# Optimization experiments

Measured on AMD Instinct MI355X. Metric: run time of the kernel, lower is better.

## Reference

```python
import jax, jax.numpy as jnp
import numpy as np

D_MODEL = 1024
NUM_HEADS = 16


def setup_inputs() -> dict:
    key = jax.random.key(0)
    ks = jax.random.split(key, 11)
    B, L, D = 1, 4096, D_MODEL
    s = 1.0 / np.sqrt(D)
    inp = {
        "Q": jax.random.normal(ks[0], (B, L, D), jnp.float32),
        "K": jax.random.normal(ks[1], (B, L, D), jnp.float32),
        "V": jax.random.normal(ks[2], (B, L, D), jnp.float32),
        "w_q": jax.random.normal(ks[3], (D, D), jnp.float32) * s,
        "b_q": jax.random.normal(ks[4], (D,), jnp.float32) * s,
        "w_k": jax.random.normal(ks[5], (D, D), jnp.float32) * s,
        "b_k": jax.random.normal(ks[6], (D,), jnp.float32) * s,
        "w_v": jax.random.normal(ks[7], (D, D), jnp.float32) * s,
        "b_v": jax.random.normal(ks[8], (D,), jnp.float32) * s,
        "w_o": jax.random.normal(ks[9], (D, D), jnp.float32) * s,
        "b_o": jax.random.normal(ks[10], (D,), jnp.float32) * s,
    }
    return inp


def _split_heads(x, n_heads):
    B, L, D = x.shape
    return x.reshape(B, L, n_heads, D // n_heads).transpose(0, 2, 1, 3)  # (B,H,L,Dh)


def reference(Q, K, V, w_q, b_q, w_k, b_k, w_v, b_v, w_o, b_o):
    H = NUM_HEADS
    # QKV projections (torch Linear: x @ W.T + b)
    q = _split_heads(Q @ w_q.T + b_q, H)
    k = _split_heads(K @ w_k.T + b_k, H)
    v = _split_heads(V @ w_v.T + b_v, H)
    d_h = q.shape[-1]
    scores = jnp.einsum("bhqd,bhkd->bhqk", q, k) / jnp.sqrt(jnp.float32(d_h))
    attn = jax.nn.softmax(scores, axis=-1)
    out = jnp.einsum("bhqk,bhkd->bhqd", attn, v)  # (B,H,L,Dh)
    B, _, L, _ = out.shape
    out = out.transpose(0, 2, 1, 3).reshape(B, L, H * d_h)
    return out @ w_o.T + b_o
```

## Files before the change

### kernel.cpp

```cpp
#include <hip/hip_runtime.h>
#include <hip/hip_bf16.h>
#include <stdint.h>

#define D_MODEL 1024
#define NHEAD   16
#define DH      64

typedef __attribute__((ext_vector_type(8))) short bf16x8;
typedef __attribute__((ext_vector_type(4))) float f32x4;

__device__ __forceinline__ ushort f2bf(float f) {
    __hip_bfloat16 h = __float2bfloat16(f);
    return *reinterpret_cast<ushort*>(&h);
}

__device__ __forceinline__ void gload_lds16(const void* g, void* l) {
    __builtin_amdgcn_global_load_lds(
        (const __attribute__((address_space(1))) void*)g,
        (__attribute__((address_space(3))) void*)l, 16, 0, 0);
}

__device__ __forceinline__ bf16x8 load8f(const float* p) {
    const float4 a = *(const float4*)p;
    const float4 b = *(const float4*)(p + 4);
    bf16x8 r;
    r[0] = (short)f2bf(a.x); r[1] = (short)f2bf(a.y);
    r[2] = (short)f2bf(a.z); r[3] = (short)f2bf(a.w);
    r[4] = (short)f2bf(b.x); r[5] = (short)f2bf(b.y);
    r[6] = (short)f2bf(b.z); r[7] = (short)f2bf(b.w);
    return r;
}

__global__ __launch_bounds__(256) void cvt_w_kernel(
    const float* __restrict__ w0, const float* __restrict__ w1,
    const float* __restrict__ w2, const float* __restrict__ w3,
    ushort* __restrict__ out)
{
    const int g = blockIdx.x * 256 + threadIdx.x;
    const int m = g >> 17;
    const int off = (g & 131071) * 8;
    const float* src = (m == 0) ? w0 : (m == 1) ? w1 : (m == 2) ? w2 : w3;
    *(bf16x8*)(out + (size_t)m * 1048576 + off) = load8f(src + off);
}

__global__ __launch_bounds__(256) void cvt_x_kernel(
    const float* __restrict__ Q, const float* __restrict__ K,
    const float* __restrict__ V,
    ushort* __restrict__ Qb, ushort* __restrict__ Kb, ushort* __restrict__ Vb)
{
    const int z = blockIdx.z;
    const float* src = (z == 0) ? Q : (z == 1) ? K : V;
    ushort* dst = (z == 0) ? Qb : (z == 1) ? Kb : Vb;
    const int off = (blockIdx.x * 256 + threadIdx.x) * 8;
    *(bf16x8*)(dst + off) = load8f(src + off);
}

__device__ __forceinline__ void storeC(float*  C, size_t i, float v) { C[i] = v; }
__device__ __forceinline__ void storeC(ushort* C, size_t i, float v) { C[i] = (short)f2bf(v); }

template<int NW, bool A_F32, typename TX, typename TOUT>
__device__ __forceinline__ void gemm_core(
    const TX* __restrict__ X,
    const ushort* __restrict__ Wb,
    const float* __restrict__ Bias,
    TOUT* __restrict__ C,
    int M, int N, int K, float scale,
    short* As, short* Bs)
{
    const int tid  = threadIdx.x;
    const int w    = tid >> 6;
    const int lane = tid & 63;
    const int quad = lane >> 4;
    const int l15  = lane & 15;
    const int wr   = (NW == 4) ? (w >> 1) : (w >> 2);
    const int wc   = (NW == 4) ? (w & 1)  : (w & 3);
    const int NJ   = (NW == 4) ? 4 : 2;
    const int colw = (NW == 4) ? 64 : 32;

    int bx = blockIdx.x, by = blockIdx.y;
    if (gridDim.x == 8 && (gridDim.y & 7) == 0) {
        const int fid   = by * 8 + bx;
        const int xcd   = fid & 7;
        const int local = fid >> 3;
        const int rpx   = gridDim.y >> 3;
        by = xcd * rpx + (local >> 3);
        bx = local & 7;
    }
    const int m0 = by * 128;
    const int n0 = bx * 128;

    f32x4 acc[4][4] = {};

    for (int k0 = 0; k0 < K; k0 += 32) {
        __syncthreads();
        #pragma unroll
        for (int c = 0; c < 8 / NW; ++c) {
            int chunk = w * (8 / NW) + c;
            int row   = chunk * 16 + (lane >> 2);
            gload_lds16(Wb + (size_t)(n0 + row) * K + k0 + (lane & 3) * 8,
                        &Bs[chunk * 512]);
        }
        if constexpr (A_F32) {
            #pragma unroll
            for (int c = 0; c < 2; ++c) {
                int idx = c * 256 + tid;
                int row = idx >> 2;
                int col = (idx & 3) * 8;
                *(bf16x8*)&As[row * 32 + col] =
                    load8f((const float*)X + (size_t)(m0 + row) * K + k0 + col);
            }
        } else {
            #pragma unroll
            for (int c = 0; c < 8 / NW; ++c) {
                int chunk = w * (8 / NW) + c;
                int row   = chunk * 16 + (lane >> 2);
                gload_lds16((const ushort*)X + (size_t)(m0 + row) * K + k0 + (lane & 3) * 8,
                            &As[chunk * 512]);
            }
        }
        __syncthreads();

        bf16x8 af[4], bfr[4];
        #pragma unroll
        for (int i = 0; i < 4; ++i)
            af[i] = *(const bf16x8*)&As[(wr * 64 + i * 16 + l15) * 32 + quad * 8];
        #pragma unroll
        for (int j = 0; j < NJ; ++j)
            bfr[j] = *(const bf16x8*)&Bs[(wc * colw + j * 16 + l15) * 32 + quad * 8];
        #pragma unroll
        for (int i = 0; i < 4; ++i)
            #pragma unroll
            for (int j = 0; j < NJ; ++j)
                acc[i][j] = __builtin_amdgcn_mfma_f32_16x16x32_bf16(af[i], bfr[j], acc[i][j], 0, 0, 0);
    }

    float bias[4];
    #pragma unroll
    for (int j = 0; j < NJ; ++j)
        bias[j] = Bias[n0 + wc * colw + j * 16 + l15];

    #pragma unroll
    for (int i = 0; i < 4; ++i) {
        int row = m0 + wr * 64 + i * 16 + quad * 4;
        #pragma unroll
        for (int j = 0; j < NJ; ++j) {
            int col = n0 + wc * colw + j * 16 + l15;
            #pragma unroll
            for (int r = 0; r < 4; ++r)
                storeC(C, (size_t)(row + r) * N + col, (acc[i][j][r] + bias[j]) * scale);
        }
    }
}

__global__ __launch_bounds__(256) void qkv_proj_f32_kernel(
    const float* __restrict__ Qin, const float* __restrict__ Kin,
    const float* __restrict__ Vin,
    const ushort* __restrict__ Wb,
    const float* __restrict__ Bq, const float* __restrict__ Bk,
    const float* __restrict__ Bv,
    ushort* qo, ushort* ko, ushort* vo, int L)
{
    __shared__ short As[4096];
    __shared__ short Bs[4096];
    const int z = blockIdx.z;
    const float *X, *B; ushort* C;
    float scale = 1.0f;
    if (z == 0)      { X = Qin; B = Bq; C = qo; scale = 0.125f * 1.44269504088896f; }
    else if (z == 1) { X = Kin; B = Bk; C = ko; }
    else             { X = Vin; B = Bv; C = vo; }
    gemm_core<4, true, float, ushort>(X, Wb + (size_t)z * 1048576, B, C,
                                      L, D_MODEL, D_MODEL, scale, As, Bs);
}

__global__ __launch_bounds__(256) void qkv_proj_bf16_kernel(
    const ushort* __restrict__ Qb, const ushort* __restrict__ Kb,
    const ushort* __restrict__ Vb,
    const ushort* __restrict__ Wb,
    const float* __restrict__ Bq, const float* __restrict__ Bk,
    const float* __restrict__ Bv,
    ushort* qo, ushort* ko, ushort* vo, int L)
{
    __shared__ short As[4096];
    __shared__ short Bs[4096];
    const int z = blockIdx.z;
    const ushort *X; const float* B; ushort* C;
    float scale = 1.0f;
    if (z == 0)      { X = Qb; B = Bq; C = qo; scale = 0.125f * 1.44269504088896f; }
    else if (z == 1) { X = Kb; B = Bk; C = ko; }
    else             { X = Vb; B = Bv; C = vo; }
    gemm_core<4, false, ushort, ushort>(X, Wb + (size_t)z * 1048576, B, C,
                                        L, D_MODEL, D_MODEL, scale, As, Bs);
}

__global__ __launch_bounds__(512) void out_proj_kernel(
    const ushort* __restrict__ Xa, const ushort* __restrict__ Wb,
    const float* __restrict__ Bo, float* out, int L)
{
    __shared__ short As[4096];
    __shared__ short Bs[4096];
    gemm_core<8, false, ushort, float>(Xa, Wb + (size_t)3 * 1048576, Bo, out,
                                       L, D_MODEL, D_MODEL, 1.0f, As, Bs);
}

__global__ __launch_bounds__(512) void attn_kernel(
    const ushort* __restrict__ Qw,
    const ushort* __restrict__ Kw,
    const ushort* __restrict__ Vw,
    ushort* __restrict__ Ow, int L)
{
    __shared__ short Ks[64 * 64];
    __shared__ short Vs[64 * 64];
    __shared__ short Ps[8][16 * 64];

    const int tid  = threadIdx.x;
    const int w    = tid >> 6;
    const int lane = tid & 63;
    const int quad = lane >> 4;
    const int l15  = lane & 15;
    const int h    = blockIdx.y;
    const int q0   = blockIdx.x * 128;

    const ushort* qp = Qw + (size_t)(q0 + w * 16 + l15) * D_MODEL + h * DH + quad * 8;
    bf16x8 qf0 = *(const bf16x8*)(qp);
    bf16x8 qf1 = *(const bf16x8*)(qp + 32);

    const int kkey = tid >> 3;
    const int kc8  = tid & 7;
    const int vkey = lane;
    const int vdh  = w * 8;

    const int krswz0 = ((quad    ) ^ (l15 & 7)) * 8;
    const int krswz1 = ((quad + 4) ^ (l15 & 7)) * 8;

    f32x4 o[4] = {};
    float m_run = -3e38f, l_run = 0.f;
    const float thr = 8.0f;

    const ushort* kptr = Kw + (size_t)kkey * D_MODEL + h * DH + kc8 * 8;
    const ushort* vptr = Vw + (size_t)vkey * D_MODEL + h * DH + vdh;
    bf16x8 kreg = *(const bf16x8*)kptr;
    bf16x8 vreg = *(const bf16x8*)vptr;

    for (int key0 = 0; key0 < L; key0 += 64) {
        __syncthreads();
        *(bf16x8*)&Ks[kkey * 64 + ((kc8 ^ (kkey & 7)) * 8)] = kreg;
        #pragma unroll
        for (int i = 0; i < 8; ++i)
            Vs[(vdh + i) * 64 + (((vkey >> 3) ^ i) * 8) + (vkey & 7)] = vreg[i];
        __syncthreads();

        if (key0 + 64 < L) {
            kptr += (size_t)64 * D_MODEL;
            vptr += (size_t)64 * D_MODEL;
            kreg = *(const bf16x8*)kptr;
            vreg = *(const bf16x8*)vptr;
        }

        f32x4 st[4];
        __builtin_amdgcn_s_setprio(1);
        #pragma unroll
        for (int kt = 0; kt < 4; ++kt) {
            const int kr = (kt * 16 + l15) * 64;
            bf16x8 kf0 = *(const bf16x8*)&Ks[kr + krswz0];
            bf16x8 kf1 = *(const bf16x8*)&Ks[kr + krswz1];
            f32x4 z = {};
            z = __builtin_amdgcn_mfma_f32_16x16x32_bf16(kf0, qf0, z, 0, 0, 0);
            z = __builtin_amdgcn_mfma_f32_16x16x32_bf16(kf1, qf1, z, 0, 0, 0);
            st[kt] = z;
        }
        __builtin_amdgcn_s_setprio(0);

        float mx = st[0][0];
        #pragma unroll
        for (int kt = 0; kt < 4; ++kt)
            #pragma unroll
            for (int r = 0; r < 4; ++r)
                mx = fmaxf(mx, st[kt][r]);
        mx = fmaxf(mx, __shfl_xor(mx, 16));
        mx = fmaxf(mx, __shfl_xor(mx, 32));

        if (!__all(mx <= m_run + thr)) {
            const float mnew  = fmaxf(m_run, mx);
            const float alpha = __builtin_amdgcn_exp2f(m_run - mnew);
            m_run = mnew;
            l_run *= alpha;
            float a[4];
            #pragma unroll
            for (int r = 0; r < 4; ++r)
                a[r] = __shfl(alpha, (lane & 48) | (quad * 4 + r));
            #pragma unroll
            for (int dt = 0; dt < 4; ++dt)
                #pragma unroll
                for (int r = 0; r < 4; ++r)
                    o[dt][r] *= a[r];
        }

        float rs = 0.f;
        #pragma unroll
        for (int kt = 0; kt < 4; ++kt) {
            float p0 = __builtin_amdgcn_exp2f(st[kt][0] - m_run);
            float p1 = __builtin_amdgcn_exp2f(st[kt][1] - m_run);
            float p2 = __builtin_amdgcn_exp2f(st[kt][2] - m_run);
            float p3 = __builtin_amdgcn_exp2f(st[kt][3] - m_run);
            rs += (p0 + p1) + (p2 + p3);
            uint2 pk;
            pk.x = (uint32_t)f2bf(p0) | ((uint32_t)f2bf(p1) << 16);
            pk.y = (uint32_t)f2bf(p2) | ((uint32_t)f2bf(p3) << 16);
            const int G = kt * 2 + (quad >> 1);
            *(uint2*)&Ps[w][l15 * 64 + ((G ^ (l15 & 7)) * 8) + (quad & 1) * 4] = pk;
        }
        rs += __shfl_xor(rs, 16);
        rs += __shfl_xor(rs, 32);
        l_run += rs;

        __builtin_amdgcn_s_setprio(1);
        #pragma unroll
        for (int f = 0; f < 2; ++f) {
            bf16x8 pf = *(const bf16x8*)&Ps[w][l15 * 64 + (((f * 4 + quad) ^ (l15 & 7)) * 8)];
            #pragma unroll
            for (int dt = 0; dt < 4; ++dt) {
                bf16x8 vf = *(const bf16x8*)&Vs[(dt * 16 + l15) * 64 + (((f * 4 + quad) ^ (l15 & 7)) * 8)];
                o[dt] = __builtin_amdgcn_mfma_f32_16x16x32_bf16(pf, vf, o[dt], 0, 0, 0);
            }
        }
        __builtin_amdgcn_s_setprio(0);
    }

    const float inv = 1.f / l_run;
    #pragma unroll
    for (int r = 0; r < 4; ++r) {
        const float linv = __shfl(inv, (lane & 48) | (quad * 4 + r));
        const int row = q0 + w * 16 + quad * 4 + r;
        #pragma unroll
        for (int dt = 0; dt < 4; ++dt) {
            int col = h * DH + dt * 16 + l15;
            Ow[(size_t)row * D_MODEL + col] = (short)f2bf(o[dt][r] * linv);
        }
    }
}

extern "C" void kernel_launch(void* const* d_in, const int* in_sizes, int n_in,
                              void* d_out, int out_size, void* d_ws, size_t ws_size,
                              hipStream_t stream) {
    const float* Q   = (const float*)d_in[0];
    const float* K   = (const float*)d_in[1];
    const float* V   = (const float*)d_in[2];
    const float* w_q = (const float*)d_in[3];
    const float* b_q = (const float*)d_in[4];
    const float* w_k = (const float*)d_in[5];
    const float* b_k = (const float*)d_in[6];
    const float* w_v = (const float*)d_in[7];
    const float* b_v = (const float*)d_in[8];
    const float* w_o = (const float*)d_in[9];
    const float* b_o = (const float*)d_in[10];
    float* out = (float*)d_out;

    const int L = in_sizes[0] / D_MODEL;
    const size_t mat = (size_t)L * D_MODEL;

    ushort* Wb   = (ushort*)d_ws;
    ushort* q_ws = (ushort*)d_out;
    ushort* k_ws = q_ws + mat;
    const bool ext = ws_size >= (size_t)40 * 1024 * 1024;

    ushort *a_ws, *v_ws, *Qb = nullptr, *Kb = nullptr, *Vb = nullptr;
    if (ext) {
        Vb   = (ushort*)d_ws + 4 * 1048576;
        v_ws = Vb + mat;
        Qb   = v_ws + mat;
        Kb   = Qb + mat;
        a_ws = Vb;
    } else {
        a_ws = (ushort*)d_ws + 4 * 1048576;
        v_ws = a_ws + mat;
    }

    cvt_w_kernel<<<dim3(2048), dim3(256), 0, stream>>>(w_q, w_k, w_v, w_o, Wb);

    dim3 gqkv(D_MODEL / 128, L / 128, 3);
    if (ext) {
        cvt_x_kernel<<<dim3(2048, 1, 3), dim3(256), 0, stream>>>(Q, K, V, Qb, Kb, Vb);
        qkv_proj_bf16_kernel<<<gqkv, dim3(256), 0, stream>>>(Qb, Kb, Vb, Wb,
                                                             b_q, b_k, b_v,
                                                             q_ws, k_ws, v_ws, L);
    } else {
        qkv_proj_f32_kernel<<<gqkv, dim3(256), 0, stream>>>(Q, K, V, Wb,
                                                            b_q, b_k, b_v,
                                                            q_ws, k_ws, v_ws, L);
    }
    dim3 gattn(L / 128, NHEAD);
    attn_kernel<<<gattn, dim3(512), 0, stream>>>(q_ws, k_ws, v_ws, a_ws, L);
    dim3 gout(D_MODEL / 128, L / 128);
    out_proj_kernel<<<gout, dim3(512), 0, stream>>>(a_ws, Wb, b_o, out, L);
}
```

Before: 286.8 us.

## Double-buffer LDS tiles in bf16 projection GEMMs to overlap loads with MFMA

Adds a pipelined GEMM path for the bf16-input QKV projection and output projection. It uses two LDS buffers, issues async global-to-LDS loads for the next K tile before computing the current one, and waits with explicit vmcnt waits and barriers. The f32-input path is split into its own single-buffered function. The goal is to hide global load latency behind MFMA work, at the cost of doubled LDS use (which may lower occupancy) and fragile hand-written waitcnt counts.

```diff
diff --git a/kernel.cpp b/kernel.cpp
--- a/kernel.cpp
+++ b/kernel.cpp
@@ -58,9 +58,20 @@
 __device__ __forceinline__ void storeC(float*  C, size_t i, float v) { C[i] = v; }
 __device__ __forceinline__ void storeC(ushort* C, size_t i, float v) { C[i] = (short)f2bf(v); }
 
-template<int NW, bool A_F32, typename TX, typename TOUT>
-__device__ __forceinline__ void gemm_core(
-    const TX* __restrict__ X,
+__device__ __forceinline__ void xcd_swizzle(int& bx, int& by) {
+    if (gridDim.x == 8 && (gridDim.y & 7) == 0) {
+        const int fid   = by * 8 + bx;
+        const int xcd   = fid & 7;
+        const int local = fid >> 3;
+        const int rpx   = gridDim.y >> 3;
+        by = xcd * rpx + (local >> 3);
+        bx = local & 7;
+    }
+}
+
+template<int NW, typename TOUT>
+__device__ __forceinline__ void gemm_pipe(
+    const ushort* __restrict__ X,
     const ushort* __restrict__ Wb,
     const float* __restrict__ Bias,
     TOUT* __restrict__ C,
@@ -76,62 +87,65 @@
     const int wc   = (NW == 4) ? (w & 1)  : (w & 3);
     const int NJ   = (NW == 4) ? 4 : 2;
     const int colw = (NW == 4) ? 64 : 32;
+    const int CH   = 8 / NW;
 
     int bx = blockIdx.x, by = blockIdx.y;
-    if (gridDim.x == 8 && (gridDim.y & 7) == 0) {
-        const int fid   = by * 8 + bx;
-        const int xcd   = fid & 7;
-        const int local = fid >> 3;
-        const int rpx   = gridDim.y >> 3;
-        by = xcd * rpx + (local >> 3);
-        bx = local & 7;
-    }
+    xcd_swizzle(bx, by);
     const int m0 = by * 128;
     const int n0 = bx * 128;
 
+    const int rin  = lane >> 2;
+    const int col8 = (lane & 3) * 8;
+
     f32x4 acc[4][4] = {};
 
-    for (int k0 = 0; k0 < K; k0 += 32) {
-        __syncthreads();
-        #pragma unroll
-        for (int c = 0; c < 8 / NW; ++c) {
-            int chunk = w * (8 / NW) + c;
-            int row   = chunk * 16 + (lane >> 2);
-            gload_lds16(Wb + (size_t)(n0 + row) * K + k0 + (lane & 3) * 8,
-                        &Bs[chunk * 512]);
-        }
-        if constexpr (A_F32) {
-            #pragma unroll
-            for (int c = 0; c < 2; ++c) {
-                int idx = c * 256 + tid;
-                int row = idx >> 2;
-                int col = (idx & 3) * 8;
-                *(bf16x8*)&As[row * 32 + col] =
-                    load8f((const float*)X + (size_t)(m0 + row) * K + k0 + col);
-            }
+    auto stage = [&](int buf, int k0) {
+        #pragma unroll
+        for (int c = 0; c < CH; ++c) {
+            int chunk = w * CH + c;
+            int row   = chunk * 16 + rin;
+            gload_lds16(Wb + (size_t)(n0 + row) * K + k0 + col8,
+                        &Bs[buf * 4096 + chunk * 512]);
+        }
+        #pragma unroll
+        for (int c = 0; c < CH; ++c) {
+            int chunk = w * CH + c;
+            int row   = chunk * 16 + rin;
+            gload_lds16(X + (size_t)(m0 + row) * K + k0 + col8,
+                        &As[buf * 4096 + chunk * 512]);
+        }
+    };
+
+    const int NT = K >> 5;
+    stage(0, 0);
+    int buf = 0;
+    for (int t = 0; t < NT; ++t) {
+        if (t + 1 < NT) {
+            stage(buf ^ 1, (t + 1) << 5);
+            if constexpr (NW == 4) asm volatile("s_waitcnt vmcnt(4)" ::: "memory");
+            else                   asm volatile("s_waitcnt vmcnt(2)" ::: "memory");
         } else {
-            #pragma unroll
-            for (int c = 0; c < 8 / NW; ++c) {
-                int chunk = w * (8 / NW) + c;
-                int row   = chunk * 16 + (lane >> 2);
-                gload_lds16((const ushort*)X + (size_t)(m0 + row) * K + k0 + (lane & 3) * 8,
-                            &As[chunk * 512]);
-            }
-        }
-        __syncthreads();
+            asm volatile("s_waitcnt vmcnt(0)" ::: "memory");
+        }
+        __builtin_amdgcn_s_barrier();
+        asm volatile("" ::: "memory");
 
         bf16x8 af[4], bfr[4];
         #pragma unroll
         for (int i = 0; i < 4; ++i)
-            af[i] = *(const bf16x8*)&As[(wr * 64 + i * 16 + l15) * 32 + quad * 8];
+            af[i] = *(const bf16x8*)&As[buf * 4096 + (wr * 64 + i * 16 + l15) * 32 + quad * 8];
         #pragma unroll
         for (int j = 0; j < NJ; ++j)
-            bfr[j] = *(const bf16x8*)&Bs[(wc * colw + j * 16 + l15) * 32 + quad * 8];
+            bfr[j] = *(const bf16x8*)&Bs[buf * 4096 + (wc * colw + j * 16 + l15) * 32 + quad * 8];
         #pragma unroll
         for (int i = 0; i < 4; ++i)
             #pragma unroll
             for (int j = 0; j < NJ; ++j)
                 acc[i][j] = __builtin_amdgcn_mfma_f32_16x16x32_bf16(af[i], bfr[j], acc[i][j], 0, 0, 0);
+
+        asm volatile("s_waitcnt lgkmcnt(0)" ::: "memory");
+        __builtin_amdgcn_s_barrier();
+        buf ^= 1;
     }
 
     float bias[4];
@@ -145,6 +159,79 @@
         #pragma unroll
         for (int j = 0; j < NJ; ++j) {
             int col = n0 + wc * colw + j * 16 + l15;
+            #pragma unroll
+            for (int r = 0; r < 4; ++r)
+                storeC(C, (size_t)(row + r) * N + col, (acc[i][j][r] + bias[j]) * scale);
+        }
+    }
+}
+
+__device__ __forceinline__ void gemm_core_f32(
+    const float* __restrict__ X,
+    const ushort* __restrict__ Wb,
+    const float* __restrict__ Bias,
+    ushort* __restrict__ C,
+    int M, int N, int K, float scale,
+    short* As, short* Bs)
+{
+    const int tid  = threadIdx.x;
+    const int w    = tid >> 6;
+    const int lane = tid & 63;
+    const int quad = lane >> 4;
+    const int l15  = lane & 15;
+    const int wr   = w >> 1, wc = w & 1;
+
+    int bx = blockIdx.x, by = blockIdx.y;
+    xcd_swizzle(bx, by);
+    const int m0 = by * 128;
+    const int n0 = bx * 128;
+
+    f32x4 acc[4][4] = {};
+
+    for (int k0 = 0; k0 < K; k0 += 32) {
+        __syncthreads();
+        #pragma unroll
+        for (int c = 0; c < 2; ++c) {
+            int chunk = w * 2 + c;
+            int row   = chunk * 16 + (lane >> 2);
+            gload_lds16(Wb + (size_t)(n0 + row) * K + k0 + (lane & 3) * 8,
+                        &Bs[chunk * 512]);
+        }
+        #pragma unroll
+        for (int c = 0; c < 2; ++c) {
+            int idx = c * 256 + tid;
+            int row = idx >> 2;
+            int col = (idx & 3) * 8;
+            *(bf16x8*)&As[row * 32 + col] =
+                load8f(X + (size_t)(m0 + row) * K + k0 + col);
+        }
+        __syncthreads();
+
+        bf16x8 af[4], bfr[4];
+        #pragma unroll
+        for (int i = 0; i < 4; ++i)
+            af[i] = *(const bf16x8*)&As[(wr * 64 + i * 16 + l15) * 32 + quad * 8];
+        #pragma unroll
+        for (int j = 0; j < 4; ++j)
+            bfr[j] = *(const bf16x8*)&Bs[(wc * 64 + j * 16 + l15) * 32 + quad * 8];
+        #pragma unroll
+        for (int i = 0; i < 4; ++i)
+            #pragma unroll
+            for (int j = 0; j < 4; ++j)
+                acc[i][j] = __builtin_amdgcn_mfma_f32_16x16x32_bf16(af[i], bfr[j], acc[i][j], 0, 0, 0);
+    }
+
+    float bias[4];
+    #pragma unroll
+    for (int j = 0; j < 4; ++j)
+        bias[j] = Bias[n0 + wc * 64 + j * 16 + l15];
+
+    #pragma unroll
+    for (int i = 0; i < 4; ++i) {
+        int row = m0 + wr * 64 + i * 16 + quad * 4;
+        #pragma unroll
+        for (int j = 0; j < 4; ++j) {
+            int col = n0 + wc * 64 + j * 16 + l15;
             #pragma unroll
             for (int r = 0; r < 4; ++r)
                 storeC(C, (size_t)(row + r) * N + col, (acc[i][j][r] + bias[j]) * scale);
@@ -168,8 +255,8 @@
     if (z == 0)      { X = Qin; B = Bq; C = qo; scale = 0.125f * 1.44269504088896f; }
     else if (z == 1) { X = Kin; B = Bk; C = ko; }
     else             { X = Vin; B = Bv; C = vo; }
-    gemm_core<4, true, float, ushort>(X, Wb + (size_t)z * 1048576, B, C,
-                                      L, D_MODEL, D_MODEL, scale, As, Bs);
+    gemm_core_f32(X, Wb + (size_t)z * 1048576, B, C,
+                  L, D_MODEL, D_MODEL, scale, As, Bs);
 }
 
 __global__ __launch_bounds__(256) void qkv_proj_bf16_kernel(
@@ -180,26 +267,26 @@
     const float* __restrict__ Bv,
     ushort* qo, ushort* ko, ushort* vo, int L)
 {
-    __shared__ short As[4096];
-    __shared__ short Bs[4096];
+    __shared__ short As[2 * 4096];
+    __shared__ short Bs[2 * 4096];
     const int z = blockIdx.z;
     const ushort *X; const float* B; ushort* C;
     float scale = 1.0f;
     if (z == 0)      { X = Qb; B = Bq; C = qo; scale = 0.125f * 1.44269504088896f; }
     else if (z == 1) { X = Kb; B = Bk; C = ko; }
     else             { X = Vb; B = Bv; C = vo; }
-    gemm_core<4, false, ushort, ushort>(X, Wb + (size_t)z * 1048576, B, C,
-                                        L, D_MODEL, D_MODEL, scale, As, Bs);
+    gemm_pipe<4, ushort>(X, Wb + (size_t)z * 1048576, B, C,
+                         L, D_MODEL, D_MODEL, scale, As, Bs);
 }
 
 __global__ __launch_bounds__(512) void out_proj_kernel(
     const ushort* __restrict__ Xa, const ushort* __restrict__ Wb,
     const float* __restrict__ Bo, float* out, int L)
 {
-    __shared__ short As[4096];
-    __shared__ short Bs[4096];
-    gemm_core<8, false, ushort, float>(Xa, Wb + (size_t)3 * 1048576, Bo, out,
-                                       L, D_MODEL, D_MODEL, 1.0f, As, Bs);
+    __shared__ short As[2 * 4096];
+    __shared__ short Bs[2 * 4096];
+    gemm_pipe<8, float>(Xa, Wb + (size_t)3 * 1048576, Bo, out,
+                        L, D_MODEL, D_MODEL, 1.0f, As, Bs);
 }
 
 __global__ __launch_bounds__(512) void attn_kernel(
```

After: 288.3 us. No clear change (+0.5%).

## Process 128 keys per attention iteration and fuse weight/input conversion kernels

Applied to the files above, without the earlier changes.

The attention kernel now stages 128 keys per loop iteration instead of 64, which halves the number of block barriers and the online-softmax rescale checks per key. It also moves the row-sum shuffle reduction out of the loop to the end. Separately, the weight and activation fp32-to-bf16 conversions are merged into one launch when the large workspace is available, removing one kernel launch. The cost is doubled K/V shared memory and more registers for the scores and prefetch, which may lower occupancy.

```diff
diff --git a/kernel.cpp b/kernel.cpp
--- a/kernel.cpp
+++ b/kernel.cpp
@@ -43,20 +43,45 @@
     *(bf16x8*)(out + (size_t)m * 1048576 + off) = load8f(src + off);
 }
 
-__global__ __launch_bounds__(256) void cvt_x_kernel(
-    const float* __restrict__ Q, const float* __restrict__ K,
-    const float* __restrict__ V,
-    ushort* __restrict__ Qb, ushort* __restrict__ Kb, ushort* __restrict__ Vb)
-{
-    const int z = blockIdx.z;
-    const float* src = (z == 0) ? Q : (z == 1) ? K : V;
-    ushort* dst = (z == 0) ? Qb : (z == 1) ? Kb : Vb;
-    const int off = (blockIdx.x * 256 + threadIdx.x) * 8;
-    *(bf16x8*)(dst + off) = load8f(src + off);
+__global__ __launch_bounds__(256) void cvt_all_kernel(
+    const float* __restrict__ w0, const float* __restrict__ w1,
+    const float* __restrict__ w2, const float* __restrict__ w3,
+    const float* __restrict__ X0, const float* __restrict__ X1,
+    const float* __restrict__ X2,
+    ushort* __restrict__ Wb,
+    ushort* __restrict__ Qb, ushort* __restrict__ Kb, ushort* __restrict__ Vb,
+    int igrp)
+{
+    const int g = blockIdx.x * 256 + threadIdx.x;
+    if (g < 524288) {
+        const int m = g >> 17;
+        const int off = (g & 131071) * 8;
+        const float* src = (m == 0) ? w0 : (m == 1) ? w1 : (m == 2) ? w2 : w3;
+        *(bf16x8*)(Wb + (size_t)m * 1048576 + off) = load8f(src + off);
+    } else {
+        const int g2 = g - 524288;
+        if (g2 >= 3 * igrp) return;
+        const int m = g2 / igrp;
+        const int off = (g2 - m * igrp) * 8;
+        const float* src = (m == 0) ? X0 : (m == 1) ? X1 : X2;
+        ushort* dst = (m == 0) ? Qb : (m == 1) ? Kb : Vb;
+        *(bf16x8*)(dst + off) = load8f(src + off);
+    }
 }
 
 __device__ __forceinline__ void storeC(float*  C, size_t i, float v) { C[i] = v; }
 __device__ __forceinline__ void storeC(ushort* C, size_t i, float v) { C[i] = (short)f2bf(v); }
+
+__device__ __forceinline__ void xcd_swizzle(int& bx, int& by) {
+    if (gridDim.x == 8 && (gridDim.y & 7) == 0) {
+        const int fid   = by * 8 + bx;
+        const int xcd   = fid & 7;
+        const int local = fid >> 3;
+        const int rpx   = gridDim.y >> 3;
+        by = xcd * rpx + (local >> 3);
+        bx = local & 7;
+    }
+}
 
 template<int NW, bool A_F32, typename TX, typename TOUT>
 __device__ __forceinline__ void gemm_core(
@@ -78,14 +103,7 @@
     const int colw = (NW == 4) ? 64 : 32;
 
     int bx = blockIdx.x, by = blockIdx.y;
-    if (gridDim.x == 8 && (gridDim.y & 7) == 0) {
-        const int fid   = by * 8 + bx;
-        const int xcd   = fid & 7;
-        const int local = fid >> 3;
-        const int rpx   = gridDim.y >> 3;
-        by = xcd * rpx + (local >> 3);
-        bx = local & 7;
-    }
+    xcd_swizzle(bx, by);
     const int m0 = by * 128;
     const int n0 = bx * 128;
 
@@ -208,8 +226,8 @@
     const ushort* __restrict__ Vw,
     ushort* __restrict__ Ow, int L)
 {
-    __shared__ short Ks[64 * 64];
-    __shared__ short Vs[64 * 64];
+    __shared__ short Ks[128 * 64];
+    __shared__ short Vs[64 * 128];
     __shared__ short Ps[8][16 * 64];
 
     const int tid  = threadIdx.x;
@@ -232,34 +250,46 @@
     const int krswz0 = ((quad    ) ^ (l15 & 7)) * 8;
     const int krswz1 = ((quad + 4) ^ (l15 & 7)) * 8;
 
+    const int kwofs = kkey * 64 + ((kc8 ^ (kkey & 7)) * 8);
+    const int vkb   = vkey >> 3;
+    const int vk7   = vkey & 7;
+
     f32x4 o[4] = {};
     float m_run = -3e38f, l_run = 0.f;
     const float thr = 8.0f;
 
-    const ushort* kptr = Kw + (size_t)kkey * D_MODEL + h * DH + kc8 * 8;
-    const ushort* vptr = Vw + (size_t)vkey * D_MODEL + h * DH + vdh;
-    bf16x8 kreg = *(const bf16x8*)kptr;
-    bf16x8 vreg = *(const bf16x8*)vptr;
-
-    for (int key0 = 0; key0 < L; key0 += 64) {
+    const ushort* kptr0 = Kw + (size_t)kkey * D_MODEL + h * DH + kc8 * 8;
+    const ushort* kptr1 = kptr0 + (size_t)64 * D_MODEL;
+    const ushort* vptr0 = Vw + (size_t)vkey * D_MODEL + h * DH + vdh;
+    const ushort* vptr1 = vptr0 + (size_t)64 * D_MODEL;
+    bf16x8 kreg0 = *(const bf16x8*)kptr0;
+    bf16x8 kreg1 = *(const bf16x8*)kptr1;
+    bf16x8 vreg0 = *(const bf16x8*)vptr0;
+    bf16x8 vreg1 = *(const bf16x8*)vptr1;
+
+    for (int key0 = 0; key0 < L; key0 += 128) {
         __syncthreads();
-        *(bf16x8*)&Ks[kkey * 64 + ((kc8 ^ (kkey & 7)) * 8)] = kreg;
-        #pragma unroll
-        for (int i = 0; i < 8; ++i)
-            Vs[(vdh + i) * 64 + (((vkey >> 3) ^ i) * 8) + (vkey & 7)] = vreg[i];
+        *(bf16x8*)&Ks[kwofs] = kreg0;
+        *(bf16x8*)&Ks[kwofs + 64 * 64] = kreg1;
+        #pragma unroll
+        for (int i = 0; i < 8; ++i) {
+            const int b = (vdh + i) * 128 + ((vkb ^ i) * 8) + vk7;
+            Vs[b]      = vreg0[i];
+            Vs[b + 64] = vreg1[i];
+        }
         __syncthreads();
 
-        if (key0 + 64 < L) {
-            kptr += (size_t)64 * D_MODEL;
-            vptr += (size_t)64 * D_MODEL;
-            kreg = *(const bf16x8*)kptr;
-            vreg = *(const bf16x8*)vptr;
-        }
-
-        f32x4 st[4];
+        if (key0 + 128 < L) {
+            kptr0 += (size_t)128 * D_MODEL;  kptr1 += (size_t)128 * D_MODEL;
+            vptr0 += (size_t)128 * D_MODEL;  vptr1 += (size_t)128 * D_MODEL;
+            kreg0 = *(const bf16x8*)kptr0;   kreg1 = *(const bf16x8*)kptr1;
+            vreg0 = *(const bf16x8*)vptr0;   vreg1 = *(const bf16x8*)vptr1;
+        }
+
+        f32x4 st[8];
         __builtin_amdgcn_s_setprio(1);
         #pragma unroll
-        for (int kt = 0; kt < 4; ++kt) {
+        for (int kt = 0; kt < 8; ++kt) {
             const int kr = (kt * 16 + l15) * 64;
             bf16x8 kf0 = *(const bf16x8*)&Ks[kr + krswz0];
             bf16x8 kf1 = *(const bf16x8*)&Ks[kr + krswz1];
@@ -272,7 +302,7 @@
 
         float mx = st[0][0];
         #pragma unroll
-        for (int kt = 0; kt < 4; ++kt)
+        for (int kt = 0; kt < 8; ++kt)
             #pragma unroll
             for (int r = 0; r < 4; ++r)
                 mx = fmaxf(mx, st[kt][r]);
@@ -295,37 +325,42 @@
                     o[dt][r] *= a[r];
         }
 
-        float rs = 0.f;
-        #pragma unroll
-        for (int kt = 0; kt < 4; ++kt) {
-            float p0 = __builtin_amdgcn_exp2f(st[kt][0] - m_run);
-            float p1 = __builtin_amdgcn_exp2f(st[kt][1] - m_run);
-            float p2 = __builtin_amdgcn_exp2f(st[kt][2] - m_run);
-            float p3 = __builtin_amdgcn_exp2f(st[kt][3] - m_run);
-            rs += (p0 + p1) + (p2 + p3);
-            uint2 pk;
-            pk.x = (uint32_t)f2bf(p0) | ((uint32_t)f2bf(p1) << 16);
-            pk.y = (uint32_t)f2bf(p2) | ((uint32_t)f2bf(p3) << 16);
-            const int G = kt * 2 + (quad >> 1);
-            *(uint2*)&Ps[w][l15 * 64 + ((G ^ (l15 & 7)) * 8) + (quad & 1) * 4] = pk;
-        }
-        rs += __shfl_xor(rs, 16);
-        rs += __shfl_xor(rs, 32);
-        l_run += rs;
-
-        __builtin_amdgcn_s_setprio(1);
-        #pragma unroll
-        for (int f = 0; f < 2; ++f) {
-            bf16x8 pf = *(const bf16x8*)&Ps[w][l15 * 64 + (((f * 4 + quad) ^ (l15 & 7)) * 8)];
-            #pragma unroll
-            for (int dt = 0; dt < 4; ++dt) {
-                bf16x8 vf = *(const bf16x8*)&Vs[(dt * 16 + l15) * 64 + (((f * 4 + quad) ^ (l15 & 7)) * 8)];
-                o[dt] = __builtin_amdgcn_mfma_f32_16x16x32_bf16(pf, vf, o[dt], 0, 0, 0);
+        #pragma unroll
+        for (int p = 0; p < 2; ++p) {
+            float rs = 0.f;
+            #pragma unroll
+            for (int kt = 0; kt < 4; ++kt) {
+                const f32x4 s = st[p * 4 + kt];
+                float p0 = __builtin_amdgcn_exp2f(s[0] - m_run);
+                float p1 = __builtin_amdgcn_exp2f(s[1] - m_run);
+                float p2 = __builtin_amdgcn_exp2f(s[2] - m_run);
+                float p3 = __builtin_amdgcn_exp2f(s[3] - m_run);
+                rs += (p0 + p1) + (p2 + p3);
+                uint2 pk;
+                pk.x = (uint32_t)f2bf(p0) | ((uint32_t)f2bf(p1) << 16);
+                pk.y = (uint32_t)f2bf(p2) | ((uint32_t)f2bf(p3) << 16);
+                const int G = kt * 2 + (quad >> 1);
+                *(uint2*)&Ps[w][l15 * 64 + ((G ^ (l15 & 7)) * 8) + (quad & 1) * 4] = pk;
             }
-        }
-        __builtin_amdgcn_s_setprio(0);
-    }
-
+            l_run += rs;
+
+            __builtin_amdgcn_s_setprio(1);
+            #pragma unroll
+            for (int f = 0; f < 2; ++f) {
+                bf16x8 pf = *(const bf16x8*)&Ps[w][l15 * 64 + (((f * 4 + quad) ^ (l15 & 7)) * 8)];
+                #pragma unroll
+                for (int dt = 0; dt < 4; ++dt) {
+                    bf16x8 vf = *(const bf16x8*)&Vs[(dt * 16 + l15) * 128 +
+                                                    (((f * 4 + quad) ^ (l15 & 7)) * 8) + p * 64];
+                    o[dt] = __builtin_amdgcn_mfma_f32_16x16x32_bf16(pf, vf, o[dt], 0, 0, 0);
+                }
+            }
+            __builtin_amdgcn_s_setprio(0);
+        }
+    }
+
+    l_run += __shfl_xor(l_run, 16);
+    l_run += __shfl_xor(l_run, 32);
     const float inv = 1.f / l_run;
     #pragma unroll
     for (int r = 0; r < 4; ++r) {
@@ -375,15 +410,17 @@
         v_ws = a_ws + mat;
     }
 
-    cvt_w_kernel<<<dim3(2048), dim3(256), 0, stream>>>(w_q, w_k, w_v, w_o, Wb);
-
     dim3 gqkv(D_MODEL / 128, L / 128, 3);
     if (ext) {
-        cvt_x_kernel<<<dim3(2048, 1, 3), dim3(256), 0, stream>>>(Q, K, V, Qb, Kb, Vb);
+        const int igrp = (int)(mat / 8);
+        const int total = 524288 + 3 * igrp;
+        cvt_all_kernel<<<dim3((total + 255) / 256), dim3(256), 0, stream>>>(
+            w_q, w_k, w_v, w_o, Q, K, V, Wb, Qb, Kb, Vb, igrp);
         qkv_proj_bf16_kernel<<<gqkv, dim3(256), 0, stream>>>(Qb, Kb, Vb, Wb,
                                                              b_q, b_k, b_v,
                                                              q_ws, k_ws, v_ws, L);
     } else {
+        cvt_w_kernel<<<dim3(2048), dim3(256), 0, stream>>>(w_q, w_k, w_v, w_o, Wb);
         qkv_proj_f32_kernel<<<gqkv, dim3(256), 0, stream>>>(Q, K, V, Wb,
                                                             b_q, b_k, b_v,
                                                             q_ws, k_ws, v_ws, L);
```

New measurement: 304.6 us. +6.2%, slower.
